# Kernel optimization log

Measured on AMD Instinct MI355X. Metric: run time of the kernel, lower is better.

Reference implementation:

```python
import jax, jax.numpy as jnp
import numpy as np

B = 65536
H = W = 28
K = 3
OUT_HW = H - K + 1  # 26, valid conv
FEAT = OUT_HW * OUT_HW  # 676
HID = 200
NCLS = 10


def setup_inputs() -> dict:
    key = jax.random.key(0)
    ks = jax.random.split(key, 6)
    x = jax.random.normal(ks[0], (B, H * W), dtype=jnp.float32)
    conv_w = jnp.ones((K, K), dtype=jnp.float32)  # Parameter(ones((3,3)))
    w1 = jax.random.normal(ks[1], (FEAT, HID), dtype=jnp.float32) * (1.0 / np.sqrt(FEAT))
    b1 = jnp.zeros((HID,), dtype=jnp.float32)
    w2 = jax.random.normal(ks[2], (HID, NCLS), dtype=jnp.float32) * (1.0 / np.sqrt(HID))
    b2 = jnp.zeros((NCLS,), dtype=jnp.float32)
    return {"x": x, "conv_w": conv_w, "w1": w1, "b1": b1, "w2": w2, "b2": b2}


def _forward(x, conv_w, w1, b1, w2, b2):
    img = x.reshape(-1, H, W)  # (B,28,28)
    # valid 3x3 single-channel cross-correlation (matches input[i:i+3,j:j+3]*w)
    lhs = img[:, None, :, :]          # (B,1,28,28)
    rhs = conv_w[None, None, :, :]    # (1,1,3,3)
    conv = jax.lax.conv_general_dilated(
        lhs, rhs, window_strides=(1, 1), padding="VALID",
        dimension_numbers=("NCHW", "OIHW", "NCHW"))  # (B,1,26,26)
    feat = conv.reshape(-1, FEAT)     # (B,676)
    hidden = jax.nn.relu(feat @ w1 + b1)  # (B,200)
    return hidden @ w2 + b2               # (B,10) logits


def reference(x, conv_w, w1, b1, w2, b2):
    return _forward(x, conv_w, w1, b1, w2, b2)
```

## Files before the change

### kernel.cpp

```cpp
#include <hip/hip_runtime.h>
#include <hip/hip_bf16.h>

#define BATCH   65536
#define HW      28
#define OHW     26
#define FEAT    676
#define KPAD    704
#define FPAD    712
#define HID     200
#define HPAD    224
#define NCLS    10
#define MT      16
#define NBLOCKS (BATCH / MT)

typedef __attribute__((ext_vector_type(8))) __bf16 bf16x8;
typedef __attribute__((ext_vector_type(4))) float  f32x4;

__device__ __forceinline__ unsigned int pk2(float a, float b) {
  __hip_bfloat16 ha = __float2bfloat16(a), hb = __float2bfloat16(b);
  return (unsigned int)__builtin_bit_cast(unsigned short, ha)
       | ((unsigned int)__builtin_bit_cast(unsigned short, hb) << 16);
}

__global__ __launch_bounds__(256) void prep_w1tf(const float* __restrict__ w1,
                                                 unsigned short* __restrict__ w1tf) {
  int idx = blockIdx.x * 256 + threadIdx.x;
  if (idx >= 704 * 208) return;
  int k = idx / 208;
  int n = idx - k * 208;
  float v = (k < FEAT && n < HID) ? w1[k * HID + n] : 0.f;
  int nt = n >> 4, ln = n & 15;
  int kc = k >> 5, r = k & 31, qd = r >> 3, j = r & 7;
  size_t dst = ((size_t)(kc * 13 + nt) * 64 + qd * 16 + ln) * 8 + j;
  __hip_bfloat16 h = __float2bfloat16(v);
  w1tf[dst] = __builtin_bit_cast(unsigned short, h);
}

__global__ __launch_bounds__(256) void prep_w2f(const float* __restrict__ w2,
                                                unsigned short* __restrict__ w2f) {
  int t = blockIdx.x * 256 + threadIdx.x;
  if (t >= 7 * 64 * 8) return;
  int j = t & 7, lane = (t >> 3) & 63, kc = t >> 9;
  int c = lane & 15;
  int k = kc * 32 + (lane >> 4) * 8 + j;
  float v = (c < NCLS && k < HID) ? w2[k * NCLS + c] : 0.f;
  __hip_bfloat16 h = __float2bfloat16(v);
  w2f[t] = __builtin_bit_cast(unsigned short, h);
}

template<int NT0, int NT>
__device__ __forceinline__ void gemm1_slice(
    const unsigned short (*feat)[FPAD], const unsigned short* __restrict__ w1tf,
    const float* __restrict__ b1, unsigned short (*hidT)[HPAD], int ln, int qd) {
  f32x4 acc[NT];
  #pragma unroll
  for (int t = 0; t < NT; ++t) acc[t] = (f32x4){0.f, 0.f, 0.f, 0.f};
  const int koff = qd * 8;
  for (int kc = 0; kc < 22; ++kc) {
    bf16x8 a = *(const bf16x8*)&feat[ln][kc * 32 + koff];
    #pragma unroll
    for (int t = 0; t < NT; ++t) {
      bf16x8 b = *(const bf16x8*)(w1tf + ((size_t)(kc * 13 + NT0 + t) * 64 + qd * 16 + ln) * 8);
      acc[t] = __builtin_amdgcn_mfma_f32_16x16x32_bf16(a, b, acc[t], 0, 0, 0);
    }
  }
  #pragma unroll
  for (int t = 0; t < NT; ++t) {
    const int n = (NT0 + t) * 16 + ln;
    if (n < HID) {
      const float bias = b1[n];
      #pragma unroll
      for (int rr = 0; rr < 4; ++rr) {
        const int m = qd * 4 + rr;
        float h = fmaxf(acc[t][rr] + bias, 0.f);
        __hip_bfloat16 hb = __float2bfloat16(h);
        hidT[m][n] = __builtin_bit_cast(unsigned short, hb);
      }
    }
  }
}

__global__ __launch_bounds__(256, 3) void fused2(
    const float* __restrict__ x, const float* __restrict__ cwp,
    const unsigned short* __restrict__ w1tf, const unsigned short* __restrict__ w2f,
    const float* __restrict__ b1, const float* __restrict__ b2,
    float* __restrict__ out) {
  __shared__ float xs[4 * 784 + 8];
  __shared__ unsigned short feat[MT][FPAD];
  __shared__ unsigned short hidT[MT][HPAD];
  const int tid  = threadIdx.x;
  const int wave = tid >> 6;
  const int lane = tid & 63;
  const int ln   = lane & 15;
  const int qd   = lane >> 4;

  for (int i = tid; i < MT * 14; i += 256) {
    int m = i / 14, d = i - m * 14;
    ((unsigned int*)&feat[0][0])[m * (FPAD / 2) + 338 + d] = 0u;
  }
  for (int i = tid; i < MT * 12; i += 256) {
    int m = i / 12, d = i - m * 12;
    ((unsigned int*)&hidT[0][0])[m * (HPAD / 2) + 100 + d] = 0u;
  }

  float cw[9];
  #pragma unroll
  for (int t = 0; t < 9; ++t) cw[t] = cwp[t];

  for (int p = 0; p < 4; ++p) {
    __syncthreads();
    const float4* xg = (const float4*)x + ((size_t)blockIdx.x * MT + 4 * p) * 196;
    float4* xs4 = (float4*)xs;
    for (int idx = tid; idx < 784; idx += 256) xs4[idx] = xg[idx];
    __syncthreads();

    const int m = 4 * p + wave;
    const float* xw = xs + wave * 784;
    #pragma unroll
    for (int it = 0; it < 2; ++it) {
      const int t = it * 64 + lane;
      if (t < 91) {
        const int iq = (t * 9363) >> 16;
        const int jc = t - 7 * iq;
        float in[4][6];
        #pragma unroll
        for (int rr = 0; rr < 4; ++rr) {
          const float* rp = xw + (2 * iq + rr) * HW + 4 * jc;
          float4 v = *(const float4*)rp;
          float2 u = *(const float2*)(rp + 4);
          in[rr][0] = v.x; in[rr][1] = v.y; in[rr][2] = v.z; in[rr][3] = v.w;
          in[rr][4] = u.x; in[rr][5] = u.y;
        }
        float o[2][4];
        #pragma unroll
        for (int dr = 0; dr < 2; ++dr)
          #pragma unroll
          for (int dc = 0; dc < 4; ++dc) {
            float s = 0.f;
            #pragma unroll
            for (int di = 0; di < 3; ++di)
              #pragma unroll
              for (int dj = 0; dj < 3; ++dj)
                s += cw[di * 3 + dj] * in[dr + di][dc + dj];
            o[dr][dc] = s;
          }
        unsigned short* fr = &feat[m][0];
        const int e0 = 52 * iq + 4 * jc;
        if (jc < 6) {
          *(uint2*)&fr[e0] = make_uint2(pk2(o[0][0], o[0][1]), pk2(o[0][2], o[0][3]));
          *(unsigned int*)&fr[e0 + OHW]     = pk2(o[1][0], o[1][1]);
          *(unsigned int*)&fr[e0 + OHW + 2] = pk2(o[1][2], o[1][3]);
        } else {
          *(unsigned int*)&fr[e0]       = pk2(o[0][0], o[0][1]);
          *(unsigned int*)&fr[e0 + OHW] = pk2(o[1][0], o[1][1]);
        }
      }
    }
  }
  __syncthreads();

  switch (wave) {
    case 0:  gemm1_slice<0, 4>(feat, w1tf, b1, hidT, ln, qd); break;
    case 1:  gemm1_slice<4, 3>(feat, w1tf, b1, hidT, ln, qd); break;
    case 2:  gemm1_slice<7, 3>(feat, w1tf, b1, hidT, ln, qd); break;
    default: gemm1_slice<10, 3>(feat, w1tf, b1, hidT, ln, qd); break;
  }
  __syncthreads();

  if (wave == 0) {
    f32x4 acc2 = (f32x4){0.f, 0.f, 0.f, 0.f};
    #pragma unroll
    for (int kc = 0; kc < 7; ++kc) {
      bf16x8 a = *(const bf16x8*)&hidT[ln][kc * 32 + qd * 8];
      bf16x8 b = *(const bf16x8*)(w2f + ((size_t)kc * 64 + lane) * 8);
      acc2 = __builtin_amdgcn_mfma_f32_16x16x32_bf16(a, b, acc2, 0, 0, 0);
    }
    if (ln < NCLS) {
      const float bb = b2[ln];
      #pragma unroll
      for (int rr = 0; rr < 4; ++rr) {
        const int m = qd * 4 + rr;
        out[((size_t)blockIdx.x * MT + m) * NCLS + ln] = acc2[rr] + bb;
      }
    }
  }
}

extern "C" void kernel_launch(void* const* d_in, const int* in_sizes, int n_in,
                              void* d_out, int out_size, void* d_ws, size_t ws_size,
                              hipStream_t stream) {
  const float* x  = (const float*)d_in[0];
  const float* cw = (const float*)d_in[1];
  const float* w1 = (const float*)d_in[2];
  const float* b1 = (const float*)d_in[3];
  const float* w2 = (const float*)d_in[4];
  const float* b2 = (const float*)d_in[5];
  float* out = (float*)d_out;

  unsigned short* w1tf = (unsigned short*)d_ws;
  unsigned short* w2f  = (unsigned short*)((char*)d_ws + 294912);

  hipLaunchKernelGGL(prep_w1tf, dim3((704 * 208 + 255) / 256), dim3(256), 0, stream,
                     w1, w1tf);
  hipLaunchKernelGGL(prep_w2f, dim3(14), dim3(256), 0, stream, w2, w2f);
  hipLaunchKernelGGL(fused2, dim3(NBLOCKS), dim3(256), 0, stream,
                     x, cw, w1tf, w2f, b1, b2, out);
}
```

Measured before the change: 356.4 us.

## Read conv input directly from global, use swizzled MFMA-fragment LDS layout

Drops the staged shared-memory copy of x and its four-phase barrier loop. Each lane now reads its conv tile straight from global memory, with the image index folded into one flat loop. Feature and hidden activations are stored in LDS in a fragment-major layout with an XOR swizzle, so the A-operand reads are contiguous 16-byte per-lane loads. The smaller LDS footprint allows raising the occupancy hint from 3 to 5 blocks per CU, at the cost of uncoalesced, overlapping global loads for the conv halo and extra index arithmetic.

```diff
diff --git a/kernel.cpp b/kernel.cpp
--- a/kernel.cpp
+++ b/kernel.cpp
@@ -5,10 +5,7 @@
 #define HW      28
 #define OHW     26
 #define FEAT    676
-#define KPAD    704
-#define FPAD    712
 #define HID     200
-#define HPAD    224
 #define NCLS    10
 #define MT      16
 #define NBLOCKS (BATCH / MT)
@@ -20,6 +17,11 @@
   __hip_bfloat16 ha = __float2bfloat16(a), hb = __float2bfloat16(b);
   return (unsigned int)__builtin_bit_cast(unsigned short, ha)
        | ((unsigned int)__builtin_bit_cast(unsigned short, hb) << 16);
+}
+
+__device__ __forceinline__ unsigned short* fslot(unsigned short* base, int m, int k) {
+  const int kc = k >> 5;
+  return base + ((kc * 64 + ((k >> 3) & 3) * 16 + (m ^ (kc & 7))) * 8) + (k & 7);
 }
 
 __global__ __launch_bounds__(256) void prep_w1tf(const float* __restrict__ w1,
@@ -50,17 +52,17 @@
 
 template<int NT0, int NT>
 __device__ __forceinline__ void gemm1_slice(
-    const unsigned short (*feat)[FPAD], const unsigned short* __restrict__ w1tf,
-    const float* __restrict__ b1, unsigned short (*hidT)[HPAD], int ln, int qd) {
+    const unsigned short* featA, const unsigned short* __restrict__ w1tf,
+    const float* __restrict__ b1, unsigned short* hidA, int lane) {
+  const int ln = lane & 15, qd = lane >> 4;
   f32x4 acc[NT];
   #pragma unroll
   for (int t = 0; t < NT; ++t) acc[t] = (f32x4){0.f, 0.f, 0.f, 0.f};
-  const int koff = qd * 8;
   for (int kc = 0; kc < 22; ++kc) {
-    bf16x8 a = *(const bf16x8*)&feat[ln][kc * 32 + koff];
+    bf16x8 a = *(const bf16x8*)&featA[(kc * 64 + (lane ^ (kc & 7))) * 8];
     #pragma unroll
     for (int t = 0; t < NT; ++t) {
-      bf16x8 b = *(const bf16x8*)(w1tf + ((size_t)(kc * 13 + NT0 + t) * 64 + qd * 16 + ln) * 8);
+      bf16x8 b = *(const bf16x8*)(w1tf + ((size_t)(kc * 13 + NT0 + t) * 64 + lane) * 8);
       acc[t] = __builtin_amdgcn_mfma_f32_16x16x32_bf16(a, b, acc[t], 0, 0, 0);
     }
   }
@@ -69,109 +71,104 @@
     const int n = (NT0 + t) * 16 + ln;
     if (n < HID) {
       const float bias = b1[n];
+      const int kc2 = n >> 5, qd2 = (n >> 3) & 3, j2 = n & 7, c2 = kc2 & 7;
       #pragma unroll
       for (int rr = 0; rr < 4; ++rr) {
         const int m = qd * 4 + rr;
         float h = fmaxf(acc[t][rr] + bias, 0.f);
         __hip_bfloat16 hb = __float2bfloat16(h);
-        hidT[m][n] = __builtin_bit_cast(unsigned short, hb);
-      }
-    }
-  }
-}
-
-__global__ __launch_bounds__(256, 3) void fused2(
+        hidA[(kc2 * 64 + qd2 * 16 + (m ^ c2)) * 8 + j2] =
+            __builtin_bit_cast(unsigned short, hb);
+      }
+    }
+  }
+}
+
+__global__ __launch_bounds__(256, 5) void fused2(
     const float* __restrict__ x, const float* __restrict__ cwp,
     const unsigned short* __restrict__ w1tf, const unsigned short* __restrict__ w2f,
     const float* __restrict__ b1, const float* __restrict__ b2,
     float* __restrict__ out) {
-  __shared__ float xs[4 * 784 + 8];
-  __shared__ unsigned short feat[MT][FPAD];
-  __shared__ unsigned short hidT[MT][HPAD];
+  __shared__ __align__(16) unsigned short featA[22 * 64 * 8];
+  __shared__ __align__(16) unsigned short hidA [ 7 * 64 * 8];
   const int tid  = threadIdx.x;
   const int wave = tid >> 6;
   const int lane = tid & 63;
-  const int ln   = lane & 15;
-  const int qd   = lane >> 4;
 
   for (int i = tid; i < MT * 14; i += 256) {
     int m = i / 14, d = i - m * 14;
-    ((unsigned int*)&feat[0][0])[m * (FPAD / 2) + 338 + d] = 0u;
+    *(unsigned int*)fslot(featA, m, 676 + 2 * d) = 0u;
   }
   for (int i = tid; i < MT * 12; i += 256) {
     int m = i / 12, d = i - m * 12;
-    ((unsigned int*)&hidT[0][0])[m * (HPAD / 2) + 100 + d] = 0u;
+    *(unsigned int*)fslot(hidA, m, 200 + 2 * d) = 0u;
   }
 
   float cw[9];
   #pragma unroll
   for (int t = 0; t < 9; ++t) cw[t] = cwp[t];
 
-  for (int p = 0; p < 4; ++p) {
-    __syncthreads();
-    const float4* xg = (const float4*)x + ((size_t)blockIdx.x * MT + 4 * p) * 196;
-    float4* xs4 = (float4*)xs;
-    for (int idx = tid; idx < 784; idx += 256) xs4[idx] = xg[idx];
-    __syncthreads();
-
-    const int m = 4 * p + wave;
-    const float* xw = xs + wave * 784;
-    #pragma unroll
-    for (int it = 0; it < 2; ++it) {
-      const int t = it * 64 + lane;
-      if (t < 91) {
-        const int iq = (t * 9363) >> 16;
-        const int jc = t - 7 * iq;
-        float in[4][6];
+  const float* xb = x + (size_t)blockIdx.x * (MT * 784);
+  for (int t0 = 0; t0 < 364; t0 += 64) {
+    const int t = t0 + lane;
+    if (t < 364) {
+      const int p   = (t * 721) >> 16;
+      const int r91 = t - 91 * p;
+      const int iq  = (r91 * 9363) >> 16;
+      const int jc  = r91 - 7 * iq;
+      const int m   = 4 * p + wave;
+      const float* xw = xb + m * 784;
+      float in[4][6];
+      const int c2 = (jc < 6) ? 4 : 2;
+      #pragma unroll
+      for (int rr = 0; rr < 4; ++rr) {
+        const float* rp = xw + (2 * iq + rr) * HW + 4 * jc;
+        const float4 v = *(const float4*)rp;
+        const float2 u = *(const float2*)(rp + c2);
+        in[rr][0] = v.x; in[rr][1] = v.y; in[rr][2] = v.z; in[rr][3] = v.w;
+        in[rr][4] = u.x; in[rr][5] = u.y;
+      }
+      float o[2][4];
+      #pragma unroll
+      for (int dr = 0; dr < 2; ++dr)
         #pragma unroll
-        for (int rr = 0; rr < 4; ++rr) {
-          const float* rp = xw + (2 * iq + rr) * HW + 4 * jc;
-          float4 v = *(const float4*)rp;
-          float2 u = *(const float2*)(rp + 4);
-          in[rr][0] = v.x; in[rr][1] = v.y; in[rr][2] = v.z; in[rr][3] = v.w;
-          in[rr][4] = u.x; in[rr][5] = u.y;
+        for (int dc = 0; dc < 4; ++dc) {
+          float s = 0.f;
+          #pragma unroll
+          for (int di = 0; di < 3; ++di)
+            #pragma unroll
+            for (int dj = 0; dj < 3; ++dj)
+              s += cw[di * 3 + dj] * in[dr + di][dc + dj];
+          o[dr][dc] = s;
         }
-        float o[2][4];
-        #pragma unroll
-        for (int dr = 0; dr < 2; ++dr)
-          #pragma unroll
-          for (int dc = 0; dc < 4; ++dc) {
-            float s = 0.f;
-            #pragma unroll
-            for (int di = 0; di < 3; ++di)
-              #pragma unroll
-              for (int dj = 0; dj < 3; ++dj)
-                s += cw[di * 3 + dj] * in[dr + di][dc + dj];
-            o[dr][dc] = s;
-          }
-        unsigned short* fr = &feat[m][0];
-        const int e0 = 52 * iq + 4 * jc;
-        if (jc < 6) {
-          *(uint2*)&fr[e0] = make_uint2(pk2(o[0][0], o[0][1]), pk2(o[0][2], o[0][3]));
-          *(unsigned int*)&fr[e0 + OHW]     = pk2(o[1][0], o[1][1]);
-          *(unsigned int*)&fr[e0 + OHW + 2] = pk2(o[1][2], o[1][3]);
-        } else {
-          *(unsigned int*)&fr[e0]       = pk2(o[0][0], o[0][1]);
-          *(unsigned int*)&fr[e0 + OHW] = pk2(o[1][0], o[1][1]);
-        }
+      const int k0 = 52 * iq + 4 * jc;
+      if (jc < 6) {
+        *(uint2*)fslot(featA, m, k0) =
+            make_uint2(pk2(o[0][0], o[0][1]), pk2(o[0][2], o[0][3]));
+        *(unsigned int*)fslot(featA, m, k0 + OHW)     = pk2(o[1][0], o[1][1]);
+        *(unsigned int*)fslot(featA, m, k0 + OHW + 2) = pk2(o[1][2], o[1][3]);
+      } else {
+        *(unsigned int*)fslot(featA, m, k0)       = pk2(o[0][0], o[0][1]);
+        *(unsigned int*)fslot(featA, m, k0 + OHW) = pk2(o[1][0], o[1][1]);
       }
     }
   }
   __syncthreads();
 
   switch (wave) {
-    case 0:  gemm1_slice<0, 4>(feat, w1tf, b1, hidT, ln, qd); break;
-    case 1:  gemm1_slice<4, 3>(feat, w1tf, b1, hidT, ln, qd); break;
-    case 2:  gemm1_slice<7, 3>(feat, w1tf, b1, hidT, ln, qd); break;
-    default: gemm1_slice<10, 3>(feat, w1tf, b1, hidT, ln, qd); break;
+    case 0:  gemm1_slice<0, 4>(featA, w1tf, b1, hidA, lane); break;
+    case 1:  gemm1_slice<4, 3>(featA, w1tf, b1, hidA, lane); break;
+    case 2:  gemm1_slice<7, 3>(featA, w1tf, b1, hidA, lane); break;
+    default: gemm1_slice<10, 3>(featA, w1tf, b1, hidA, lane); break;
   }
   __syncthreads();
 
   if (wave == 0) {
+    const int ln = lane & 15, qd = lane >> 4;
     f32x4 acc2 = (f32x4){0.f, 0.f, 0.f, 0.f};
     #pragma unroll
     for (int kc = 0; kc < 7; ++kc) {
-      bf16x8 a = *(const bf16x8*)&hidT[ln][kc * 32 + qd * 8];
+      bf16x8 a = *(const bf16x8*)&hidA[(kc * 64 + (lane ^ (kc & 7))) * 8];
       bf16x8 b = *(const bf16x8*)(w2f + ((size_t)kc * 64 + lane) * 8);
       acc2 = __builtin_amdgcn_mfma_f32_16x16x32_bf16(a, b, acc2, 0, 0, 0);
     }
@@ -179,8 +176,7 @@
       const float bb = b2[ln];
       #pragma unroll
       for (int rr = 0; rr < 4; ++rr) {
-        const int m = qd * 4 + rr;
-        out[((size_t)blockIdx.x * MT + m) * NCLS + ln] = acc2[rr] + bb;
+        out[((size_t)blockIdx.x * MT + qd * 4 + rr) * NCLS + ln] = acc2[rr] + bb;
       }
     }
   }
```

New measurement: 355.4 us. No clear change (-0.3%).
